# Performance work log

Hardware: AMD Instinct MI355X
Metric: run time of the kernel (lower is better)

The kernel has to match this reference:

```python
import jax, jax.numpy as jnp
import numpy as np

OGF_H, OGF_W = 256, 704
DOWNSAMPLE = 16
FH, FW = OGF_H // DOWNSAMPLE, OGF_W // DOWNSAMPLE  # 16, 44
D_BINS = 41  # len(arange(4.0, 45.0, 1.0))
NUM_C_TRANS = 128
NX, NY, NZ = 128, 128, 1  # from x/y/z bounds
DX = jnp.array([0.8, 0.8, 20.0], jnp.float32)
BX = jnp.array([-50.8, -50.8, 0.0], jnp.float32)  # lower + dx/2


def make_frustum():
    # (D, fH, fW, 3) pixel-coordinate frustum: (u, v, depth)
    ds = jnp.arange(4.0, 45.0, 1.0, dtype=jnp.float32)[:, None, None] * jnp.ones((1, FH, FW), jnp.float32)
    xs = jnp.linspace(0.0, OGF_W - 1.0, FW, dtype=jnp.float32)[None, None, :] * jnp.ones((D_BINS, FH, 1), jnp.float32)
    ys = jnp.linspace(0.0, OGF_H - 1.0, FH, dtype=jnp.float32)[None, :, None] * jnp.ones((D_BINS, 1, FW), jnp.float32)
    return jnp.stack([xs, ys, ds], axis=-1)


def setup_inputs() -> dict:
    key = jax.random.key(0)
    k = jax.random.split(key, 4)
    B, N, Cin = 1, 6, 512
    x = jax.random.normal(k[0], (B, N, Cin, FH, FW), jnp.float32)
    # camera->ego rotation: ego_x = cam_z (depth), ego_y = cam_x, ego_z = -cam_y
    R = jnp.array([[0.0, 0.0, 1.0], [1.0, 0.0, 0.0], [0.0, -1.0, 0.0]], jnp.float32)
    rots = jnp.broadcast_to(R, (B, N, 3, 3)).copy()
    trans = jax.random.uniform(k[1], (B, N, 3), jnp.float32, -2.0, 2.0)
    fx, fy, cx, cy = 552.0, 552.0, OGF_W / 2.0, OGF_H / 2.0
    K = jnp.array([[fx, 0.0, cx], [0.0, fy, cy], [0.0, 0.0, 1.0]], jnp.float32)
    intrins = jnp.broadcast_to(K, (B, N, 3, 3)).copy()
    post_rots = jnp.broadcast_to(jnp.eye(3, dtype=jnp.float32), (B, N, 3, 3)).copy()
    post_trans = jnp.zeros((B, N, 3), jnp.float32)
    # 1x1 conv == matmul over channels: weight (D + C_trans, Cin), bias (D + C_trans,)
    w_depth = jax.random.normal(k[2], (D_BINS + NUM_C_TRANS, Cin), jnp.float32) * 0.02
    b_depth = jax.random.normal(k[3], (D_BINS + NUM_C_TRANS,), jnp.float32) * 0.02
    return {"x": x, "rots": rots, "trans": trans, "intrins": intrins,
            "post_rots": post_rots, "post_trans": post_trans,
            "w_depth": w_depth, "b_depth": b_depth}


def _forward(x, rots, trans, intrins, post_rots, post_trans, w_depth, b_depth):
    B, N, Cin, H, W = x.shape
    frustum = make_frustum()  # (D, H, W, 3)

    # ---- get_geometry ----
    inv_post = jnp.linalg.inv(post_rots)      # (B,N,3,3)
    inv_intr = jnp.linalg.inv(intrins)        # (B,N,3,3)
    pts = frustum[None, None] - post_trans[:, :, None, None, None, :]          # (B,N,D,H,W,3)
    pts = jnp.einsum('bnij,bndhwj->bndhwi', inv_post, pts)
    pts = jnp.concatenate([pts[..., :2] * pts[..., 2:3], pts[..., 2:3]], axis=-1)
    combine = jnp.einsum('bnij,bnjk->bnik', rots, inv_intr)
    geom = jnp.einsum('bnij,bndhwj->bndhwi', combine, pts) + trans[:, :, None, None, None, :]

    # ---- get_volume: 1x1 conv -> depth softmax x feature outer product ----
    feat = jnp.einsum('oc,bnchw->bnohw', w_depth, x) + b_depth[None, None, :, None, None]
    depth = jax.nn.softmax(feat[:, :, :D_BINS], axis=2)          # (B,N,D,H,W)
    cfeat = feat[:, :, D_BINS:D_BINS + NUM_C_TRANS]              # (B,N,C,H,W)
    vol = depth[:, :, None] * cfeat[:, :, :, None]               # (B,N,C,D,H,W)
    vol = jnp.transpose(vol, (0, 1, 3, 4, 5, 2))                 # (B,N,D,H,W,C)

    # ---- voxel_pooling via segment_sum (== sort + cumsum-trick + scatter) ----
    gi = ((geom - (BX - DX / 2.0)) / DX).astype(jnp.int32)       # trunc-toward-zero, matches .long()
    Nprime = B * N * D_BINS * H * W
    gi = gi.reshape(B, Nprime // B, 3)
    valid = ((gi[..., 0] >= 0) & (gi[..., 0] < NX) &
             (gi[..., 1] >= 0) & (gi[..., 1] < NY) &
             (gi[..., 2] >= 0) & (gi[..., 2] < NZ))               # (B, Nprime//B)
    batch_ix = jnp.arange(B, dtype=jnp.int32)[:, None]
    ranks = (gi[..., 0] * (NY * NZ * B) + gi[..., 1] * (NZ * B)
             + gi[..., 2] * B + batch_ix)
    nseg = NX * NY * NZ * B
    ranks = jnp.where(valid, ranks, nseg).reshape(-1)             # OOB ids dropped by segment_sum
    vol_flat = jnp.where(valid.reshape(-1)[:, None], vol.reshape(Nprime, NUM_C_TRANS), 0.0)
    seg = jax.ops.segment_sum(vol_flat, ranks, num_segments=nseg)  # (nx*ny*nz*B, C)
    # rank layout = ((ix*NY + iy)*NZ + iz)*B + b  ->  (NX, NY, NZ, B, C)
    final = seg.reshape(NX, NY, NZ, B, NUM_C_TRANS)
    final = jnp.transpose(final, (3, 2, 4, 1, 0))                 # (B, nz, C, ny, nx)
    # torch.cat(final.unbind(dim=2), 1): z-major channel stacking
    return final.reshape(B, NZ * NUM_C_TRANS, NY, NX)


def reference(x, rots, trans, intrins, post_rots, post_trans, w_depth, b_depth):
    return _forward(x, rots, trans, intrins, post_rots, post_trans, w_depth, b_depth)
```

## Files before the change

### kernel.cpp

```cpp
#include <hip/hip_runtime.h>
#include <math.h>

#define FHH 16
#define FWW 44
#define DB 41
#define NCAM 6
#define CIN 512
#define NC 128
#define NPIX (FHH*FWW)
#define TOTPIX (NCAM*NPIX)
#define NPTS (NCAM*DB*NPIX)
#define NSPAT (128*128)
#define CHUNK 128
#define MOUT 169
#define PARTSZ (NCAM*MOUT*NPIX)

#define OFF_MATS   0
#define OFF_BINS   256
#define OFF_PLIST  (OFF_BINS + NPTS)
#define OFF_WLIST  (OFF_PLIST + NPTS)
#define OFF_PART   (OFF_WLIST + NPTS)
#define OFF_TMP    OFF_PART
#define OFF_FEATD  (OFF_PART + 4*PARTSZ)
#define OFF_CFEATT (OFF_FEATD + NCAM*DB*NPIX)
#define OFF_OFFS   (OFF_CFEATT + TOTPIX*NC)
#define OFF_CNT    (OFF_OFFS + 16400)
#define OFF_CNT2   (OFF_CNT + NSPAT)

__device__ void lapack_inv3(const float* src, float* dst) {
    float A[3][3]; int piv[3];
    for (int i = 0; i < 3; i++)
        for (int j = 0; j < 3; j++) A[i][j] = src[i*3+j];
    for (int j = 0; j < 3; j++) {
        int p = j; float mx = fabsf(A[j][j]);
        for (int i = j+1; i < 3; i++) { float v = fabsf(A[i][j]); if (v > mx) { mx = v; p = i; } }
        piv[j] = p;
        if (p != j) for (int k = 0; k < 3; k++) { float t = A[j][k]; A[j][k] = A[p][k]; A[p][k] = t; }
        float r = __fdiv_rn(1.0f, A[j][j]);
        for (int i = j+1; i < 3; i++) A[i][j] = __fmul_rn(A[i][j], r);
        for (int i = j+1; i < 3; i++)
            for (int k = j+1; k < 3; k++)
                A[i][k] = __fsub_rn(A[i][k], __fmul_rn(A[i][j], A[j][k]));
    }
    for (int j = 0; j < 3; j++) {
        float ajj = __fdiv_rn(1.0f, A[j][j]);
        A[j][j] = ajj;
        float najj = -ajj;
        for (int k = 0; k < j; k++) {
            float temp = A[k][j];
            for (int i = 0; i < k; i++) A[i][j] = __fadd_rn(A[i][j], __fmul_rn(temp, A[i][k]));
            A[k][j] = __fmul_rn(temp, A[k][k]);
        }
        for (int i = 0; i < j; i++) A[i][j] = __fmul_rn(A[i][j], najj);
    }
    float work[3];
    for (int j = 2; j >= 0; j--) {
        for (int i = j+1; i < 3; i++) { work[i] = A[i][j]; A[i][j] = 0.0f; }
        for (int k = j+1; k < 3; k++) {
            float t = -work[k];
            for (int i = 0; i < 3; i++) A[i][j] = __fadd_rn(A[i][j], __fmul_rn(t, A[i][k]));
        }
    }
    for (int j = 2; j >= 0; j--) {
        int p = piv[j];
        if (p != j) for (int i = 0; i < 3; i++) { float t = A[i][j]; A[i][j] = A[i][p]; A[i][p] = t; }
    }
    for (int i = 0; i < 3; i++)
        for (int j = 0; j < 3; j++) dst[i*3+j] = A[i][j];
}

__global__ void prep_kernel(const float* __restrict__ rots, const float* __restrict__ intrins,
                            const float* __restrict__ post_rots, float* __restrict__ mats) {
    int n = threadIdx.x;
    if (n >= NCAM) return;
    float invK[9], invP[9], M[9];
    lapack_inv3(intrins + n*9, invK);
    lapack_inv3(post_rots + n*9, invP);
    for (int i = 0; i < 3; i++)
        for (int k = 0; k < 3; k++) {
            float s = __fmul_rn(rots[n*9 + i*3 + 0], invK[0*3 + k]);
            s = __fadd_rn(s, __fmul_rn(rots[n*9 + i*3 + 1], invK[1*3 + k]));
            s = __fadd_rn(s, __fmul_rn(rots[n*9 + i*3 + 2], invK[2*3 + k]));
            M[i*3 + k] = s;
        }
    for (int i = 0; i < 9; i++) { mats[n*18 + i] = M[i]; mats[n*18 + 9 + i] = invP[i]; }
}

__global__ void bins_kernel(const float* __restrict__ trans, const float* __restrict__ post_trans,
                            const float* __restrict__ mats, int* __restrict__ bins,
                            int* __restrict__ cnt) {
    int p = blockIdx.x * 256 + threadIdx.x;
    int pc = p < NPTS ? p : NPTS - 1;
    int n   = pc / (DB*NPIX);
    int rem = pc % (DB*NPIX);
    int d   = rem / NPIX;
    int pix = rem % NPIX;
    int h = pix / FWW, w = pix % FWW;
    float xs = (float)((double)w * (703.0/43.0));
    float ys = (float)((double)h * (255.0/15.0));
    float ds = 4.0f + (float)d;
    const float* M = mats + n*18;
    const float* P = mats + n*18 + 9;
    float px = __fsub_rn(xs, post_trans[n*3+0]);
    float py = __fsub_rn(ys, post_trans[n*3+1]);
    float pz = __fsub_rn(ds, post_trans[n*3+2]);
    float q0 = __fadd_rn(__fadd_rn(__fmul_rn(P[0],px), __fmul_rn(P[1],py)), __fmul_rn(P[2],pz));
    float q1 = __fadd_rn(__fadd_rn(__fmul_rn(P[3],px), __fmul_rn(P[4],py)), __fmul_rn(P[5],pz));
    float q2 = __fadd_rn(__fadd_rn(__fmul_rn(P[6],px), __fmul_rn(P[7],py)), __fmul_rn(P[8],pz));
    float r0 = __fmul_rn(q0, q2);
    float r1 = __fmul_rn(q1, q2);
    float r2 = q2;
    float g0 = __fadd_rn(__fadd_rn(__fadd_rn(__fmul_rn(M[0],r0), __fmul_rn(M[1],r1)), __fmul_rn(M[2],r2)), trans[n*3+0]);
    float g1 = __fadd_rn(__fadd_rn(__fadd_rn(__fmul_rn(M[3],r0), __fmul_rn(M[4],r1)), __fmul_rn(M[5],r2)), trans[n*3+1]);
    float g2 = __fadd_rn(__fadd_rn(__fadd_rn(__fmul_rn(M[6],r0), __fmul_rn(M[7],r1)), __fmul_rn(M[8],r2)), trans[n*3+2]);
    const float lox = -50.8f - (0.8f/2.0f);
    const float loy = -50.8f - (0.8f/2.0f);
    const float loz =   0.0f - (20.0f/2.0f);
    int gx = (int)(__fdiv_rn(__fsub_rn(g0, lox), 0.8f));
    int gy = (int)(__fdiv_rn(__fsub_rn(g1, loy), 0.8f));
    int gz = (int)(__fdiv_rn(__fsub_rn(g2, loz), 20.0f));
    bool ok = (gx >= 0) & (gx < 128) & (gy >= 0) & (gy < 128) & (gz >= 0) & (gz < 1);
    int s = ok ? (gy*128 + gx) : -1;
    if (p < NPTS) bins[p] = s;
    bool valid = (p < NPTS) && (s >= 0);
    int lane = threadIdx.x & 63;
    unsigned long long todo = __ballot(valid);
    while (todo) {
        int lead = __builtin_ctzll(todo);
        int ls = __shfl(s, lead);
        unsigned long long match = __ballot(valid && (s == ls));
        if (valid && (s == ls)) {
            unsigned long long ltmask = (1ull << lane) - 1ull;
            int rank = __popcll(match & ltmask);
            if (rank == 0) atomicAdd(&cnt[ls], __popcll(match));
        }
        todo &= ~match;
    }
}

#define KT 16
__global__ __launch_bounds__(256) void feat_part(const float* __restrict__ x,
                                                 const float* __restrict__ wd,
                                                 float* __restrict__ part) {
    __shared__ float xsm[KT][64];
    __shared__ float wt[KT][64];
    int n   = blockIdx.z >> 2;
    int ksp = blockIdx.z & 3;
    int o0 = blockIdx.y * 64;
    int p0 = blockIdx.x * 64;
    int tid = threadIdx.x;
    int tx = tid & 15;
    int ty = tid >> 4;
    const float* xbase = x + (size_t)n * CIN * NPIX + p0;

    int lk  = tid >> 4;
    int px4 = (tid & 15) * 4;
    int lo  = tid & 63;
    int lkq = tid >> 6;
    int orow = min(o0 + lo, MOUT - 1);

    float acc[4][4];
    #pragma unroll
    for (int i = 0; i < 4; i++)
        #pragma unroll
        for (int j = 0; j < 4; j++) acc[i][j] = 0.0f;

    int cbeg = ksp * 128;
    for (int c0 = cbeg; c0 < cbeg + 128; c0 += KT) {
        float4 xv = *(const float4*)(xbase + (size_t)(c0 + lk) * NPIX + px4);
        float4 wv = *(const float4*)(wd + (size_t)orow * CIN + c0 + lkq * 4);
        *(float4*)&xsm[lk][px4] = xv;
        wt[lkq*4 + 0][lo] = wv.x;
        wt[lkq*4 + 1][lo] = wv.y;
        wt[lkq*4 + 2][lo] = wv.z;
        wt[lkq*4 + 3][lo] = wv.w;
        __syncthreads();
        #pragma unroll
        for (int k = 0; k < KT; k++) {
            float4 a = *(const float4*)&xsm[k][tx*4];
            float4 b = *(const float4*)&wt[k][ty*4];
            acc[0][0] = fmaf(b.x, a.x, acc[0][0]);
            acc[0][1] = fmaf(b.x, a.y, acc[0][1]);
            acc[0][2] = fmaf(b.x, a.z, acc[0][2]);
            acc[0][3] = fmaf(b.x, a.w, acc[0][3]);
            acc[1][0] = fmaf(b.y, a.x, acc[1][0]);
            acc[1][1] = fmaf(b.y, a.y, acc[1][1]);
            acc[1][2] = fmaf(b.y, a.z, acc[1][2]);
            acc[1][3] = fmaf(b.y, a.w, acc[1][3]);
            acc[2][0] = fmaf(b.z, a.x, acc[2][0]);
            acc[2][1] = fmaf(b.z, a.y, acc[2][1]);
            acc[2][2] = fmaf(b.z, a.z, acc[2][2]);
            acc[2][3] = fmaf(b.z, a.w, acc[2][3]);
            acc[3][0] = fmaf(b.w, a.x, acc[3][0]);
            acc[3][1] = fmaf(b.w, a.y, acc[3][1]);
            acc[3][2] = fmaf(b.w, a.z, acc[3][2]);
            acc[3][3] = fmaf(b.w, a.w, acc[3][3]);
        }
        __syncthreads();
    }

    float* pb = part + ((size_t)(ksp * NCAM + n) * MOUT) * NPIX + p0 + tx*4;
    #pragma unroll
    for (int i = 0; i < 4; i++) {
        int o = ty*4 + i + o0;
        if (o >= MOUT) continue;
        float4 v = make_float4(acc[i][0], acc[i][1], acc[i][2], acc[i][3]);
        *(float4*)(pb + (size_t)o * NPIX) = v;
    }
}

#define RPIX 32
__global__ __launch_bounds__(128) void fuse_kernel(const float* __restrict__ part,
                                                   const float* __restrict__ bd,
                                                   float* __restrict__ featd,
                                                   float* __restrict__ cfeatT) {
    __shared__ float red[8][RPIX];
    __shared__ float ctile[RPIX][129];
    int px = threadIdx.x & 31;
    int ty = threadIdx.x >> 5;
    int gpix = blockIdx.x * RPIX + px;
    int n  = gpix / NPIX;
    int pp = gpix % NPIX;
    const float* pbase = part + ((size_t)n * MOUT) * NPIX + pp;

    float v[43];
    #pragma unroll
    for (int i = 0; i < 43; i++) {
        int o = ty + 4*i;
        if (o < MOUT) {
            const float* p = pbase + (size_t)o * NPIX;
            float s = __fadd_rn(__fadd_rn(__fadd_rn(p[0], p[PARTSZ]), p[2*PARTSZ]), p[3*PARTSZ]);
            v[i] = __fadd_rn(s, bd[o]);
        }
    }
    float pmax = -1e30f;
    #pragma unroll
    for (int i = 0; i < 43; i++) { int o = ty + 4*i; if (o < DB) pmax = fmaxf(pmax, v[i]); }
    red[ty][px] = pmax;
    __syncthreads();
    float m = fmaxf(fmaxf(red[0][px], red[1][px]), fmaxf(red[2][px], red[3][px]));
    float psum = 0.0f;
    #pragma unroll
    for (int i = 0; i < 43; i++) {
        int o = ty + 4*i;
        if (o < DB) { v[i] = expf(v[i] - m); psum += v[i]; }
    }
    red[4 + ty][px] = psum;
    __syncthreads();
    float tot = __fadd_rn(__fadd_rn(__fadd_rn(red[4][px], red[5][px]), red[6][px]), red[7][px]);
    float inv = __fdiv_rn(1.0f, tot);
    #pragma unroll
    for (int i = 0; i < 43; i++) {
        int o = ty + 4*i;
        if (o < DB)        featd[((size_t)n * DB + o) * NPIX + pp] = __fmul_rn(v[i], inv);
        else if (o < MOUT) ctile[px][o - DB] = v[i];
    }
    __syncthreads();
    int pixbase = blockIdx.x * RPIX;
    #pragma unroll
    for (int r = 0; r < 32; r++) {
        int idx = threadIdx.x + 128 * r;
        int row = idx >> 7;
        int c   = idx & 127;
        cfeatT[(size_t)(pixbase + row) * NC + c] = ctile[row][c];
    }
}

__global__ void scan_kernel(const int* __restrict__ cnt, int* __restrict__ offsets) {
    __shared__ int sums[1024];
    int t = threadIdx.x;
    int vals[16];
    int run = 0;
    #pragma unroll
    for (int i = 0; i < 16; i++) { vals[i] = cnt[t*16 + i]; run += vals[i]; }
    sums[t] = run;
    __syncthreads();
    for (int off = 1; off < 1024; off <<= 1) {
        int u = (t >= off) ? sums[t - off] : 0;
        __syncthreads();
        sums[t] += u;
        __syncthreads();
    }
    int base = (t == 0) ? 0 : sums[t - 1];
    #pragma unroll
    for (int i = 0; i < 16; i++) { offsets[t*16 + i] = base; base += vals[i]; }
    if (t == 1023) offsets[NSPAT] = base;
}

__global__ void fill_kernel(const int* __restrict__ bins, const float* __restrict__ featd,
                            const int* __restrict__ offsets, int* __restrict__ cnt2,
                            int* __restrict__ plist, float* __restrict__ wlist) {
    int p = blockIdx.x * 256 + threadIdx.x;
    int pc = p < NPTS ? p : NPTS - 1;
    int s = bins[pc];
    bool valid = (p < NPTS) && (s >= 0);
    int n   = pc / (DB*NPIX);
    int rem = pc % (DB*NPIX);
    int d   = rem / NPIX;
    int pix = rem % NPIX;
    int lane = threadIdx.x & 63;
    int pos = 0;
    unsigned long long todo = __ballot(valid);
    while (todo) {
        int lead = __builtin_ctzll(todo);
        int ls = __shfl(s, lead);
        unsigned long long match = __ballot(valid && (s == ls));
        if (valid && (s == ls)) {
            unsigned long long ltmask = (1ull << lane) - 1ull;
            int rank = __popcll(match & ltmask);
            int basep = 0;
            if (rank == 0) basep = atomicAdd(&cnt2[ls], __popcll(match));
            basep = __shfl(basep, lead);
            pos = offsets[ls] + basep + rank;
        }
        todo &= ~match;
    }
    if (valid) {
        float w = featd[((size_t)n * DB + d) * NPIX + pix];
        plist[pos] = (s << 13) | (n * NPIX + pix);
        wlist[pos] = w;
    }
}

__global__ void gather_kernel(const int* __restrict__ offsets, const int* __restrict__ plist,
                              const float* __restrict__ wlist, const float* __restrict__ cfeatT,
                              float* __restrict__ tmp) {
    __shared__ int keys[CHUNK];
    __shared__ float wts[CHUNK];
    int T = offsets[NSPAT];
    int base = blockIdx.x * CHUNK;
    if (base >= T) return;
    int end = min(base + CHUNK, T);
    int m = end - base;
    int c = threadIdx.x;
    if (c < m) { keys[c] = plist[base + c]; wts[c] = wlist[base + c]; }
    __syncthreads();
    float acc = 0.0f;
    int cur = keys[0] >> 13;
    for (int i = 0; i < m; i++) {
        int key = keys[i];
        int s = key >> 13;
        if (s != cur) {
            bool span = (offsets[cur] < base) || (offsets[cur + 1] > end);
            if (span) atomicAdd(&tmp[(size_t)cur * NC + c], acc);
            else      tmp[(size_t)cur * NC + c] = acc;
            acc = 0.0f;
            cur = s;
        }
        acc = fmaf(wts[i], cfeatT[(size_t)(key & 0x1FFF) * NC + c], acc);
    }
    bool span = (offsets[cur] < base) || (offsets[cur + 1] > end);
    if (span) atomicAdd(&tmp[(size_t)cur * NC + c], acc);
    else      tmp[(size_t)cur * NC + c] = acc;
}

__global__ void transpose_kernel(const float* __restrict__ tmp, float* __restrict__ out) {
    __shared__ float tile[32][33];
    int s0 = blockIdx.x * 32;
    int c0 = blockIdx.y * 32;
    int tx = threadIdx.x;
    int ty = threadIdx.y;
    #pragma unroll
    for (int i = 0; i < 32; i += 8)
        tile[ty + i][tx] = tmp[(size_t)(s0 + ty + i) * NC + c0 + tx];
    __syncthreads();
    #pragma unroll
    for (int i = 0; i < 32; i += 8)
        out[(size_t)(c0 + ty + i) * NSPAT + s0 + tx] = tile[tx][ty + i];
}

extern "C" void kernel_launch(void* const* d_in, const int* in_sizes, int n_in,
                              void* d_out, int out_size, void* d_ws, size_t ws_size,
                              hipStream_t stream) {
    const float* x          = (const float*)d_in[0];
    const float* rots       = (const float*)d_in[1];
    const float* trans      = (const float*)d_in[2];
    const float* intrins    = (const float*)d_in[3];
    const float* post_rots  = (const float*)d_in[4];
    const float* post_trans = (const float*)d_in[5];
    const float* w_depth    = (const float*)d_in[6];
    const float* b_depth    = (const float*)d_in[7];
    float* out = (float*)d_out;
    float* ws  = (float*)d_ws;

    float* mats    = ws + OFF_MATS;
    int*   bins    = (int*)(ws + OFF_BINS);
    int*   plist   = (int*)(ws + OFF_PLIST);
    float* wlist   = ws + OFF_WLIST;
    float* part    = ws + OFF_PART;
    float* featd   = ws + OFF_FEATD;
    float* cfeatT  = ws + OFF_CFEATT;
    int*   offsets = (int*)(ws + OFF_OFFS);
    int*   cnt     = (int*)(ws + OFF_CNT);
    int*   cnt2    = (int*)(ws + OFF_CNT2);
    float* tmp     = ws + OFF_TMP;

    hipMemsetAsync(cnt, 0, 2 * NSPAT * sizeof(int), stream);
    prep_kernel<<<1, 64, 0, stream>>>(rots, intrins, post_rots, mats);
    bins_kernel<<<(NPTS + 255) / 256, 256, 0, stream>>>(trans, post_trans, mats, bins, cnt);
    feat_part<<<dim3(11, 3, NCAM * 4), 256, 0, stream>>>(x, w_depth, part);
    fuse_kernel<<<TOTPIX / RPIX, 128, 0, stream>>>(part, b_depth, featd, cfeatT);
    scan_kernel<<<1, 1024, 0, stream>>>(cnt, offsets);
    fill_kernel<<<(NPTS + 255) / 256, 256, 0, stream>>>(bins, featd, offsets, cnt2, plist, wlist);
    hipMemsetAsync(tmp, 0, (size_t)NSPAT * NC * sizeof(float), stream);
    gather_kernel<<<(NPTS + CHUNK - 1) / CHUNK, NC, 0, stream>>>(offsets, plist, wlist, cfeatT, tmp);
    transpose_kernel<<<dim3(NSPAT / 32, NC / 32), dim3(32, 8), 0, stream>>>(tmp, out);
}
```

Measured before the change: 190.2 us.

## Shard bin-count atomics, fold prep into bins kernel, merge memsets

Per-cell atomic counters are split into four shards keyed by wavefront index, which spreads atomic contention on hot BEV cells across more addresses. The scan and offsets are expanded to match, and the gather keeps per-cell boundaries by reading shard 0 of consecutive cells. The separate camera-matrix prep kernel is folded into the bins kernel, where every block recomputes it into shared memory. The workspace is reordered so a single memset zeroes the counters and the accumulation buffer together. The cost is a scan four times larger and redundant per-block matrix inversion.

```diff
diff --git a/kernel.cpp b/kernel.cpp
--- a/kernel.cpp
+++ b/kernel.cpp
@@ -14,18 +14,19 @@
 #define CHUNK 128
 #define MOUT 169
 #define PARTSZ (NCAM*MOUT*NPIX)
-
-#define OFF_MATS   0
-#define OFF_BINS   256
+#define NS 4
+
+#define OFF_CNT    0
+#define OFF_CNT2   (NSPAT*NS)
+#define OFF_TMP    (2*NSPAT*NS)
+#define ZERO_FLOATS (2*NSPAT*NS + NSPAT*NC)
+#define OFF_OFFS   ZERO_FLOATS
+#define OFF_BINS   (OFF_OFFS + NSPAT*NS + 16)
 #define OFF_PLIST  (OFF_BINS + NPTS)
 #define OFF_WLIST  (OFF_PLIST + NPTS)
 #define OFF_PART   (OFF_WLIST + NPTS)
-#define OFF_TMP    OFF_PART
 #define OFF_FEATD  (OFF_PART + 4*PARTSZ)
 #define OFF_CFEATT (OFF_FEATD + NCAM*DB*NPIX)
-#define OFF_OFFS   (OFF_CFEATT + TOTPIX*NC)
-#define OFF_CNT    (OFF_OFFS + 16400)
-#define OFF_CNT2   (OFF_CNT + NSPAT)
 
 __device__ void lapack_inv3(const float* src, float* dst) {
     float A[3][3]; int piv[3];
@@ -69,26 +70,31 @@
         for (int j = 0; j < 3; j++) dst[i*3+j] = A[i][j];
 }
 
-__global__ void prep_kernel(const float* __restrict__ rots, const float* __restrict__ intrins,
-                            const float* __restrict__ post_rots, float* __restrict__ mats) {
-    int n = threadIdx.x;
-    if (n >= NCAM) return;
-    float invK[9], invP[9], M[9];
-    lapack_inv3(intrins + n*9, invK);
-    lapack_inv3(post_rots + n*9, invP);
-    for (int i = 0; i < 3; i++)
-        for (int k = 0; k < 3; k++) {
-            float s = __fmul_rn(rots[n*9 + i*3 + 0], invK[0*3 + k]);
-            s = __fadd_rn(s, __fmul_rn(rots[n*9 + i*3 + 1], invK[1*3 + k]));
-            s = __fadd_rn(s, __fmul_rn(rots[n*9 + i*3 + 2], invK[2*3 + k]));
-            M[i*3 + k] = s;
-        }
-    for (int i = 0; i < 9; i++) { mats[n*18 + i] = M[i]; mats[n*18 + 9 + i] = invP[i]; }
-}
-
-__global__ void bins_kernel(const float* __restrict__ trans, const float* __restrict__ post_trans,
-                            const float* __restrict__ mats, int* __restrict__ bins,
-                            int* __restrict__ cnt) {
+__global__ __launch_bounds__(256) void bins_kernel(const float* __restrict__ rots,
+                                                   const float* __restrict__ intrins,
+                                                   const float* __restrict__ post_rots,
+                                                   const float* __restrict__ trans,
+                                                   const float* __restrict__ post_trans,
+                                                   int* __restrict__ bins,
+                                                   int* __restrict__ cnt4) {
+    __shared__ float sM[NCAM*9], sP[NCAM*9], sT[NCAM*3], sPT[NCAM*3];
+    if (threadIdx.x < NCAM) {
+        int nn = threadIdx.x;
+        float invK[9], invP[9];
+        lapack_inv3(intrins + nn*9, invK);
+        lapack_inv3(post_rots + nn*9, invP);
+        for (int i = 0; i < 3; i++)
+            for (int k = 0; k < 3; k++) {
+                float s = __fmul_rn(rots[nn*9 + i*3 + 0], invK[0*3 + k]);
+                s = __fadd_rn(s, __fmul_rn(rots[nn*9 + i*3 + 1], invK[1*3 + k]));
+                s = __fadd_rn(s, __fmul_rn(rots[nn*9 + i*3 + 2], invK[2*3 + k]));
+                sM[nn*9 + i*3 + k] = s;
+            }
+        for (int i = 0; i < 9; i++) sP[nn*9 + i] = invP[i];
+        for (int i = 0; i < 3; i++) { sT[nn*3 + i] = trans[nn*3 + i]; sPT[nn*3 + i] = post_trans[nn*3 + i]; }
+    }
+    __syncthreads();
+
     int p = blockIdx.x * 256 + threadIdx.x;
     int pc = p < NPTS ? p : NPTS - 1;
     int n   = pc / (DB*NPIX);
@@ -99,20 +105,20 @@
     float xs = (float)((double)w * (703.0/43.0));
     float ys = (float)((double)h * (255.0/15.0));
     float ds = 4.0f + (float)d;
-    const float* M = mats + n*18;
-    const float* P = mats + n*18 + 9;
-    float px = __fsub_rn(xs, post_trans[n*3+0]);
-    float py = __fsub_rn(ys, post_trans[n*3+1]);
-    float pz = __fsub_rn(ds, post_trans[n*3+2]);
+    const float* M = sM + n*9;
+    const float* P = sP + n*9;
+    float px = __fsub_rn(xs, sPT[n*3+0]);
+    float py = __fsub_rn(ys, sPT[n*3+1]);
+    float pz = __fsub_rn(ds, sPT[n*3+2]);
     float q0 = __fadd_rn(__fadd_rn(__fmul_rn(P[0],px), __fmul_rn(P[1],py)), __fmul_rn(P[2],pz));
     float q1 = __fadd_rn(__fadd_rn(__fmul_rn(P[3],px), __fmul_rn(P[4],py)), __fmul_rn(P[5],pz));
     float q2 = __fadd_rn(__fadd_rn(__fmul_rn(P[6],px), __fmul_rn(P[7],py)), __fmul_rn(P[8],pz));
     float r0 = __fmul_rn(q0, q2);
     float r1 = __fmul_rn(q1, q2);
     float r2 = q2;
-    float g0 = __fadd_rn(__fadd_rn(__fadd_rn(__fmul_rn(M[0],r0), __fmul_rn(M[1],r1)), __fmul_rn(M[2],r2)), trans[n*3+0]);
-    float g1 = __fadd_rn(__fadd_rn(__fadd_rn(__fmul_rn(M[3],r0), __fmul_rn(M[4],r1)), __fmul_rn(M[5],r2)), trans[n*3+1]);
-    float g2 = __fadd_rn(__fadd_rn(__fadd_rn(__fmul_rn(M[6],r0), __fmul_rn(M[7],r1)), __fmul_rn(M[8],r2)), trans[n*3+2]);
+    float g0 = __fadd_rn(__fadd_rn(__fadd_rn(__fmul_rn(M[0],r0), __fmul_rn(M[1],r1)), __fmul_rn(M[2],r2)), sT[n*3+0]);
+    float g1 = __fadd_rn(__fadd_rn(__fadd_rn(__fmul_rn(M[3],r0), __fmul_rn(M[4],r1)), __fmul_rn(M[5],r2)), sT[n*3+1]);
+    float g2 = __fadd_rn(__fadd_rn(__fadd_rn(__fmul_rn(M[6],r0), __fmul_rn(M[7],r1)), __fmul_rn(M[8],r2)), sT[n*3+2]);
     const float lox = -50.8f - (0.8f/2.0f);
     const float loy = -50.8f - (0.8f/2.0f);
     const float loz =   0.0f - (20.0f/2.0f);
@@ -124,6 +130,7 @@
     if (p < NPTS) bins[p] = s;
     bool valid = (p < NPTS) && (s >= 0);
     int lane = threadIdx.x & 63;
+    int shard = (threadIdx.x >> 6) & (NS - 1);
     unsigned long long todo = __ballot(valid);
     while (todo) {
         int lead = __builtin_ctzll(todo);
@@ -132,7 +139,7 @@
         if (valid && (s == ls)) {
             unsigned long long ltmask = (1ull << lane) - 1ull;
             int rank = __popcll(match & ltmask);
-            if (rank == 0) atomicAdd(&cnt[ls], __popcll(match));
+            if (rank == 0) atomicAdd(&cnt4[ls*NS + shard], __popcll(match));
         }
         todo &= ~match;
     }
@@ -266,13 +273,13 @@
     }
 }
 
-__global__ void scan_kernel(const int* __restrict__ cnt, int* __restrict__ offsets) {
+__global__ __launch_bounds__(1024) void scan_kernel(const int* __restrict__ cnt4, int* __restrict__ offs) {
     __shared__ int sums[1024];
+    const int PER = (NSPAT * NS) / 1024;
     int t = threadIdx.x;
-    int vals[16];
+    int base_i = t * PER;
     int run = 0;
-    #pragma unroll
-    for (int i = 0; i < 16; i++) { vals[i] = cnt[t*16 + i]; run += vals[i]; }
+    for (int i = 0; i < PER; i++) run += cnt4[base_i + i];
     sums[t] = run;
     __syncthreads();
     for (int off = 1; off < 1024; off <<= 1) {
@@ -282,14 +289,14 @@
         __syncthreads();
     }
     int base = (t == 0) ? 0 : sums[t - 1];
-    #pragma unroll
-    for (int i = 0; i < 16; i++) { offsets[t*16 + i] = base; base += vals[i]; }
-    if (t == 1023) offsets[NSPAT] = base;
-}
-
-__global__ void fill_kernel(const int* __restrict__ bins, const float* __restrict__ featd,
-                            const int* __restrict__ offsets, int* __restrict__ cnt2,
-                            int* __restrict__ plist, float* __restrict__ wlist) {
+    for (int i = 0; i < PER; i++) { offs[base_i + i] = base; base += cnt4[base_i + i]; }
+    if (t == 1023) offs[NSPAT * NS] = base;
+}
+
+__global__ __launch_bounds__(256) void fill_kernel(const int* __restrict__ bins,
+                                                   const float* __restrict__ featd,
+                                                   const int* __restrict__ offs, int* __restrict__ cnt2,
+                                                   int* __restrict__ plist, float* __restrict__ wlist) {
     int p = blockIdx.x * 256 + threadIdx.x;
     int pc = p < NPTS ? p : NPTS - 1;
     int s = bins[pc];
@@ -299,6 +306,7 @@
     int d   = rem / NPIX;
     int pix = rem % NPIX;
     int lane = threadIdx.x & 63;
+    int shard = (threadIdx.x >> 6) & (NS - 1);
     int pos = 0;
     unsigned long long todo = __ballot(valid);
     while (todo) {
@@ -309,9 +317,9 @@
             unsigned long long ltmask = (1ull << lane) - 1ull;
             int rank = __popcll(match & ltmask);
             int basep = 0;
-            if (rank == 0) basep = atomicAdd(&cnt2[ls], __popcll(match));
+            if (rank == 0) basep = atomicAdd(&cnt2[ls*NS + shard], __popcll(match));
             basep = __shfl(basep, lead);
-            pos = offsets[ls] + basep + rank;
+            pos = offs[ls*NS + shard] + basep + rank;
         }
         todo &= ~match;
     }
@@ -322,12 +330,14 @@
     }
 }
 
-__global__ void gather_kernel(const int* __restrict__ offsets, const int* __restrict__ plist,
-                              const float* __restrict__ wlist, const float* __restrict__ cfeatT,
-                              float* __restrict__ tmp) {
+__global__ __launch_bounds__(128) void gather_kernel(const int* __restrict__ offs,
+                                                     const int* __restrict__ plist,
+                                                     const float* __restrict__ wlist,
+                                                     const float* __restrict__ cfeatT,
+                                                     float* __restrict__ tmp) {
     __shared__ int keys[CHUNK];
     __shared__ float wts[CHUNK];
-    int T = offsets[NSPAT];
+    int T = offs[NSPAT * NS];
     int base = blockIdx.x * CHUNK;
     if (base >= T) return;
     int end = min(base + CHUNK, T);
@@ -341,7 +351,7 @@
         int key = keys[i];
         int s = key >> 13;
         if (s != cur) {
-            bool span = (offsets[cur] < base) || (offsets[cur + 1] > end);
+            bool span = (offs[cur*NS] < base) || (offs[cur*NS + NS] > end);
             if (span) atomicAdd(&tmp[(size_t)cur * NC + c], acc);
             else      tmp[(size_t)cur * NC + c] = acc;
             acc = 0.0f;
@@ -349,7 +359,7 @@
         }
         acc = fmaf(wts[i], cfeatT[(size_t)(key & 0x1FFF) * NC + c], acc);
     }
-    bool span = (offsets[cur] < base) || (offsets[cur + 1] > end);
+    bool span = (offs[cur*NS] < base) || (offs[cur*NS + NS] > end);
     if (span) atomicAdd(&tmp[(size_t)cur * NC + c], acc);
     else      tmp[(size_t)cur * NC + c] = acc;
 }
@@ -383,26 +393,23 @@
     float* out = (float*)d_out;
     float* ws  = (float*)d_ws;
 
-    float* mats    = ws + OFF_MATS;
+    int*   cnt4    = (int*)(ws + OFF_CNT);
+    int*   cnt2    = (int*)(ws + OFF_CNT2);
+    float* tmp     = ws + OFF_TMP;
+    int*   offs    = (int*)(ws + OFF_OFFS);
     int*   bins    = (int*)(ws + OFF_BINS);
     int*   plist   = (int*)(ws + OFF_PLIST);
     float* wlist   = ws + OFF_WLIST;
     float* part    = ws + OFF_PART;
     float* featd   = ws + OFF_FEATD;
     float* cfeatT  = ws + OFF_CFEATT;
-    int*   offsets = (int*)(ws + OFF_OFFS);
-    int*   cnt     = (int*)(ws + OFF_CNT);
-    int*   cnt2    = (int*)(ws + OFF_CNT2);
-    float* tmp     = ws + OFF_TMP;
-
-    hipMemsetAsync(cnt, 0, 2 * NSPAT * sizeof(int), stream);
-    prep_kernel<<<1, 64, 0, stream>>>(rots, intrins, post_rots, mats);
-    bins_kernel<<<(NPTS + 255) / 256, 256, 0, stream>>>(trans, post_trans, mats, bins, cnt);
+
+    hipMemsetAsync(ws, 0, (size_t)ZERO_FLOATS * sizeof(float), stream);
+    bins_kernel<<<(NPTS + 255) / 256, 256, 0, stream>>>(rots, intrins, post_rots, trans, post_trans, bins, cnt4);
     feat_part<<<dim3(11, 3, NCAM * 4), 256, 0, stream>>>(x, w_depth, part);
+    scan_kernel<<<1, 1024, 0, stream>>>(cnt4, offs);
     fuse_kernel<<<TOTPIX / RPIX, 128, 0, stream>>>(part, b_depth, featd, cfeatT);
-    scan_kernel<<<1, 1024, 0, stream>>>(cnt, offsets);
-    fill_kernel<<<(NPTS + 255) / 256, 256, 0, stream>>>(bins, featd, offsets, cnt2, plist, wlist);
-    hipMemsetAsync(tmp, 0, (size_t)NSPAT * NC * sizeof(float), stream);
-    gather_kernel<<<(NPTS + CHUNK - 1) / CHUNK, NC, 0, stream>>>(offsets, plist, wlist, cfeatT, tmp);
+    fill_kernel<<<(NPTS + 255) / 256, 256, 0, stream>>>(bins, featd, offs, cnt2, plist, wlist);
+    gather_kernel<<<(NPTS + CHUNK - 1) / CHUNK, 128, 0, stream>>>(offs, plist, wlist, cfeatT, tmp);
     transpose_kernel<<<dim3(NSPAT / 32, NC / 32), dim3(32, 8), 0, stream>>>(tmp, out);
 }
```

Result: slower. 197.9 us (+4.1%).
